# Kernel optimization log

Hardware: AMD Instinct MI355X
Metric: run time of the kernel (lower is better)

The kernel has to match this reference:

```python
import jax, jax.numpy as jnp
import numpy as np

HIDDEN = 512


def setup_inputs() -> dict:
    key = jax.random.key(0)
    k1, k2, k3, k4, k5 = jax.random.split(key, 5)
    scale = 1.0 / np.sqrt(HIDDEN)
    return {
        "decoder_hidden": jax.random.normal(k1, (64, HIDDEN), dtype=jnp.float32),
        "encoder_outputs": jax.random.normal(k2, (4096, 64, HIDDEN), dtype=jnp.float32),
        "W1": jax.random.uniform(k3, (HIDDEN, HIDDEN), jnp.float32, -scale, scale),
        "W2": jax.random.uniform(k4, (HIDDEN, HIDDEN), jnp.float32, -scale, scale),
        "v": jax.random.uniform(k5, (HIDDEN,), jnp.float32, -scale, scale),
    }


def reference(decoder_hidden, encoder_outputs, W1, W2, v):
    # decoder_hidden: (B, H); encoder_outputs: (S, B, H)
    enc = jnp.transpose(encoder_outputs, (1, 0, 2))          # (B, S, H)
    dec_proj = decoder_hidden @ W1.T                          # (B, H) — no need to repeat over S
    enc_proj = jnp.einsum('bsh,gh->bsg', enc, W2)             # (B, S, H)
    energy = jnp.tanh(dec_proj[:, None, :] + enc_proj) @ v    # (B, S)
    attn_weights = jax.nn.softmax(energy, axis=1)             # (B, S)
    context = jnp.einsum('bs,bsh->bh', attn_weights, enc)     # (B, H)
    return (context, attn_weights)
```

## Files before the change

kernel.cpp:

```cpp
#include <hip/hip_runtime.h>
#include <math.h>


#define BATCH 64
#define SEQ   4096
#define HID   512

typedef __attribute__((ext_vector_type(8))) short bf16x8;
typedef __attribute__((ext_vector_type(4))) float f32x4;

__device__ __forceinline__ float fast_tanh(float x) {
    return 1.0f - 2.0f / (__expf(2.0f * x) + 1.0f);
}

__device__ __forceinline__ unsigned cvt2(float lo, float hi) {
    unsigned r;
    asm("v_cvt_pk_bf16_f32 %0, %1, %2" : "=v"(r) : "v"(lo), "v"(hi));
    return r;
}

__device__ __forceinline__ void lds_barrier() {
    asm volatile("s_waitcnt lgkmcnt(0)" ::: "memory");
    __builtin_amdgcn_s_barrier();
}

__global__ void k_cvtW2(const float* __restrict__ W2, ushort* __restrict__ W2t)
{
    const int n  = blockIdx.x * 256 + threadIdx.x;
    const int g  = n >> 6, kc = n & 63;
    const int kb = kc >> 2, rgl = kc & 3;
    const int gh = g >> 8, wv = (g >> 6) & 3, fn = (g >> 4) & 3, gl = g & 15;

    const float* src = W2 + (size_t)g * HID + kc * 8;
    const float4 x = *reinterpret_cast<const float4*>(src);
    const float4 y = *reinterpret_cast<const float4*>(src + 4);
    uint4 u;
    u.x = cvt2(x.x, x.y);  u.y = cvt2(x.z, x.w);
    u.z = cvt2(y.x, y.y);  u.w = cvt2(y.z, y.w);

    const size_t dst = (size_t)gh * 131072 + kb * 8192 + wv * 2048 + fn * 512
                     + (rgl * 16 + gl) * 8;
    *reinterpret_cast<uint4*>(W2t + dst) = u;
}

__global__ void k_decproj(const float* __restrict__ dh,
                          const float* __restrict__ W1,
                          float* __restrict__ dp)
{
    __shared__ float wrow[HID];
    const int g = blockIdx.x;
    const int t = threadIdx.x;
    for (int i = t; i < HID; i += 256) wrow[i] = W1[g * HID + i];
    __syncthreads();

    const int b = t >> 2, q = t & 3;
    const float* dhb = dh + b * HID + q * 128;
    const float* wr  = wrow + q * 128;
    float acc = 0.f;
    #pragma unroll 8
    for (int i = 0; i < 128; i += 4) {
        const float4 d4 = *reinterpret_cast<const float4*>(dhb + i);
        acc = fmaf(d4.x, wr[i + 0], acc);
        acc = fmaf(d4.y, wr[i + 1], acc);
        acc = fmaf(d4.z, wr[i + 2], acc);
        acc = fmaf(d4.w, wr[i + 3], acc);
    }
    acc += __shfl_xor(acc, 1);
    acc += __shfl_xor(acc, 2);
    if (q == 0) dp[b * HID + g] = acc;
}

#define LDA 40

__global__ __launch_bounds__(256, 4)
void k_energy(const float* __restrict__ enc, const ushort* __restrict__ W2t,
              const float* __restrict__ dp,  const float* __restrict__ v,
              float* __restrict__ eparts)
{
    __shared__ __align__(16) ushort As[2][64 * LDA];
    __shared__ float part[4][64];

    const int idx  = blockIdx.x;
    const int g16  = idx >> 4, rr = idx & 15;
    const int gh   = rr >> 3;
    const int pair = (g16 << 3) | (rr & 7);
    const int schunk = pair & 63;
    const int b      = pair >> 6;
    const int s0     = schunk * 64;

    const int t    = threadIdx.x;
    const int lane = t & 63;
    const int wv   = t >> 6;
    const int gl   = lane & 15, rg = lane >> 4;

    f32x4 acc[4][4];
    const f32x4 z = {0.f, 0.f, 0.f, 0.f};
    #pragma unroll
    for (int m = 0; m < 4; ++m)
        #pragma unroll
        for (int n = 0; n < 4; ++n) acc[m][n] = z;

    const int arow = t >> 2, akq = t & 3;
    const float* aptr = enc + ((size_t)(s0 + arow) * BATCH + b) * HID + akq * 8;
    ushort* Aw0 = &As[0][arow * LDA + akq * 8];
    ushort* Aw1 = &As[1][arow * LDA + akq * 8];

    const ushort* Ap0 = &As[0][gl * LDA + rg * 8];
    const ushort* Ap1 = &As[1][gl * LDA + rg * 8];

    const ushort* bptr = W2t + (size_t)gh * 131072 + wv * 2048 + lane * 8;

    float4 a0 = *reinterpret_cast<const float4*>(aptr);
    float4 a1 = *reinterpret_cast<const float4*>(aptr + 4);
    {
        uint4 aw;
        aw.x = cvt2(a0.x, a0.y);  aw.y = cvt2(a0.z, a0.w);
        aw.z = cvt2(a1.x, a1.y);  aw.w = cvt2(a1.z, a1.w);
        *reinterpret_cast<uint4*>(Aw0) = aw;
    }
    a0 = *reinterpret_cast<const float4*>(aptr + 32);
    a1 = *reinterpret_cast<const float4*>(aptr + 36);
    lds_barrier();

    #pragma unroll
    for (int kb = 0; kb < 16; ++kb) {
        bf16x8 bfr[4];
        #pragma unroll
        for (int n = 0; n < 4; ++n)
            bfr[n] = *reinterpret_cast<const bf16x8*>(bptr + kb * 8192 + n * 512);

        const ushort* Ap = (kb & 1) ? Ap1 : Ap0;
        bf16x8 af[4];
        #pragma unroll
        for (int m = 0; m < 4; ++m)
            af[m] = *reinterpret_cast<const bf16x8*>(Ap + m * 16 * LDA);

        if (kb < 15) {
            uint4 aw;
            aw.x = cvt2(a0.x, a0.y);  aw.y = cvt2(a0.z, a0.w);
            aw.z = cvt2(a1.x, a1.y);  aw.w = cvt2(a1.z, a1.w);
            *reinterpret_cast<uint4*>((kb & 1) ? Aw0 : Aw1) = aw;
        }
        if (kb < 14) {
            a0 = *reinterpret_cast<const float4*>(aptr + (kb + 2) * 32);
            a1 = *reinterpret_cast<const float4*>(aptr + (kb + 2) * 32 + 4);
        }

        #pragma unroll
        for (int m = 0; m < 4; ++m)
            #pragma unroll
            for (int n = 0; n < 4; ++n)
                acc[m][n] = __builtin_amdgcn_mfma_f32_16x16x32_bf16(
                    af[m], bfr[n], acc[m][n], 0, 0, 0);

        lds_barrier();
    }

    float dpv[4], vv[4];
    #pragma unroll
    for (int n = 0; n < 4; ++n) {
        const int g = gh * 256 + wv * 64 + n * 16 + gl;
        dpv[n] = dp[b * HID + g];
        vv[n]  = v[g];
    }
    float p[4][4];
    #pragma unroll
    for (int m = 0; m < 4; ++m)
        #pragma unroll
        for (int r = 0; r < 4; ++r) p[m][r] = 0.f;
    #pragma unroll
    for (int n = 0; n < 4; ++n)
        #pragma unroll
        for (int m = 0; m < 4; ++m)
            #pragma unroll
            for (int r = 0; r < 4; ++r)
                p[m][r] += fast_tanh(dpv[n] + acc[m][n][r]) * vv[n];

    #pragma unroll
    for (int m = 0; m < 4; ++m)
        #pragma unroll
        for (int r = 0; r < 4; ++r) {
            float x = p[m][r];
            x += __shfl_xor(x, 1);
            x += __shfl_xor(x, 2);
            x += __shfl_xor(x, 4);
            x += __shfl_xor(x, 8);
            p[m][r] = x;
        }
    if (gl == 0) {
        #pragma unroll
        for (int m = 0; m < 4; ++m)
            #pragma unroll
            for (int r = 0; r < 4; ++r)
                part[wv][m * 16 + rg * 4 + r] = p[m][r];
    }
    __syncthreads();

    if (t < 64) {
        const float e = part[0][t] + part[1][t] + part[2][t] + part[3][t];
        eparts[(size_t)gh * BATCH * SEQ + (size_t)b * SEQ + s0 + t] = e;
    }
}

__global__ void k_softmax(const float* __restrict__ eparts,
                          float* __restrict__ attn)
{
    __shared__ float redm[4], reds[4];
    const int b = blockIdx.x, t = threadIdx.x;
    const float* e0 = eparts + (size_t)b * SEQ;
    const float* e1 = eparts + (size_t)BATCH * SEQ + (size_t)b * SEQ;

    float4 ev[4];
    float m = -3.4e38f;
    #pragma unroll
    for (int i = 0; i < 4; ++i) {
        const float4 x = *reinterpret_cast<const float4*>(e0 + i * 1024 + t * 4);
        const float4 y = *reinterpret_cast<const float4*>(e1 + i * 1024 + t * 4);
        ev[i] = make_float4(x.x + y.x, x.y + y.y, x.z + y.z, x.w + y.w);
        m = fmaxf(m, fmaxf(fmaxf(ev[i].x, ev[i].y), fmaxf(ev[i].z, ev[i].w)));
    }
    #pragma unroll
    for (int off = 1; off < 64; off <<= 1) m = fmaxf(m, __shfl_xor(m, off));
    if ((t & 63) == 0) redm[t >> 6] = m;
    __syncthreads();
    m = fmaxf(fmaxf(redm[0], redm[1]), fmaxf(redm[2], redm[3]));

    float s = 0.f;
    #pragma unroll
    for (int i = 0; i < 4; ++i) {
        ev[i].x = __expf(ev[i].x - m);  ev[i].y = __expf(ev[i].y - m);
        ev[i].z = __expf(ev[i].z - m);  ev[i].w = __expf(ev[i].w - m);
        s += (ev[i].x + ev[i].y) + (ev[i].z + ev[i].w);
    }
    #pragma unroll
    for (int off = 1; off < 64; off <<= 1) s += __shfl_xor(s, off);
    if ((t & 63) == 0) reds[t >> 6] = s;
    __syncthreads();
    s = (reds[0] + reds[1]) + (reds[2] + reds[3]);
    const float inv = 1.0f / s;

    float* o = attn + (size_t)b * SEQ;
    #pragma unroll
    for (int i = 0; i < 4; ++i) {
        const float4 w4 = make_float4(ev[i].x * inv, ev[i].y * inv,
                                      ev[i].z * inv, ev[i].w * inv);
        *reinterpret_cast<float4*>(o + i * 1024 + t * 4) = w4;
    }
}

__global__ void k_ctxpart(const float* __restrict__ enc,
                          const float* __restrict__ attn,
                          float* __restrict__ pctx)
{
    __shared__ float w[256];
    const int b  = blockIdx.x;
    const int sp = blockIdx.y;
    const int t  = threadIdx.x;

    w[t] = attn[(size_t)b * SEQ + sp * 256 + t];
    __syncthreads();

    const float2* e2 = reinterpret_cast<const float2*>(enc);
    size_t idx = ((size_t)sp * 256 * BATCH + b) * (HID / 2) + t;
    const size_t stride = (size_t)BATCH * (HID / 2);

    float ax = 0.f, ay = 0.f;
    #pragma unroll 4
    for (int s = 0; s < 256; ++s) {
        const float2 ev = e2[idx];
        const float ws = w[s];
        ax = fmaf(ws, ev.x, ax);
        ay = fmaf(ws, ev.y, ay);
        idx += stride;
    }
    float2* p2 = reinterpret_cast<float2*>(pctx);
    p2[((size_t)sp * BATCH + b) * (HID / 2) + t] = make_float2(ax, ay);
}

__global__ void k_ctxsum(const float* __restrict__ pctx,
                         float* __restrict__ ctx)
{
    const int i = blockIdx.x * 256 + threadIdx.x;
    float s = 0.f;
    #pragma unroll
    for (int sp = 0; sp < 16; ++sp) s += pctx[(size_t)sp * BATCH * HID + i];
    ctx[i] = s;
}

extern "C" void kernel_launch(void* const* d_in, const int* in_sizes, int n_in,
                              void* d_out, int out_size, void* d_ws, size_t ws_size,
                              hipStream_t stream)
{
    const float* dh  = (const float*)d_in[0];
    const float* enc = (const float*)d_in[1];
    const float* W1  = (const float*)d_in[2];
    const float* W2  = (const float*)d_in[3];
    const float* v   = (const float*)d_in[4];

    float* out  = (float*)d_out;
    float* ctx  = out;
    float* attn = out + BATCH * HID;

    float*  dp      = (float*)d_ws;
    ushort* W2t     = (ushort*)(dp + BATCH * HID);
    float*  shared2 = (float*)(W2t + HID * HID);
    float*  eparts  = shared2;
    float*  pctx    = shared2;

    k_cvtW2  <<<128, 256, 0, stream>>>(W2, W2t);
    k_decproj<<<HID, 256, 0, stream>>>(dh, W1, dp);
    k_energy <<<8192, 256, 0, stream>>>(enc, W2t, dp, v, eparts);
    k_softmax<<<BATCH, 256, 0, stream>>>(eparts, attn);
    k_ctxpart<<<dim3(BATCH, 16), 256, 0, stream>>>(enc, attn, pctx);
    k_ctxsum <<<BATCH * HID / 256, 256, 0, stream>>>(pctx, ctx);
}
```

Measured before the change: 328.8 us.

## Software-pipeline energy GEMM with register double-buffered fragments and deeper prefetch

Restructures the k_energy main loop so the W2 fragments and LDS A fragments for the next k-block are loaded into double-buffered registers before the MFMAs of the current block run. Global prefetch of encoder rows moves one step further ahead, and the barrier now sits before the next-fragment LDS read instead of after the MFMAs. The goal is to hide global and LDS load latency behind MFMA work. The extra register buffers raise register pressure, so launch bounds drop from 4 to 3 blocks per SM, which lowers occupancy.

Measured after the change: 347.4 us. 1.06x slower.

```diff
diff --git a/kernel.cpp b/kernel.cpp
--- a/kernel.cpp
+++ b/kernel.cpp
@@ -72,7 +72,7 @@
 
 #define LDA 40
 
-__global__ __launch_bounds__(256, 4)
+__global__ __launch_bounds__(256, 3)
 void k_energy(const float* __restrict__ enc, const ushort* __restrict__ W2t,
               const float* __restrict__ dp,  const float* __restrict__ v,
               float* __restrict__ eparts)
@@ -110,40 +110,56 @@
 
     const ushort* bptr = W2t + (size_t)gh * 131072 + wv * 2048 + lane * 8;
 
-    float4 a0 = *reinterpret_cast<const float4*>(aptr);
-    float4 a1 = *reinterpret_cast<const float4*>(aptr + 4);
+    bf16x8 af[2][4], bfr[2][4];
+    float4 ar[2][2];
+
     {
+        const float4 p0 = *reinterpret_cast<const float4*>(aptr);
+        const float4 p1 = *reinterpret_cast<const float4*>(aptr + 4);
         uint4 aw;
-        aw.x = cvt2(a0.x, a0.y);  aw.y = cvt2(a0.z, a0.w);
-        aw.z = cvt2(a1.x, a1.y);  aw.w = cvt2(a1.z, a1.w);
+        aw.x = cvt2(p0.x, p0.y);  aw.y = cvt2(p0.z, p0.w);
+        aw.z = cvt2(p1.x, p1.y);  aw.w = cvt2(p1.z, p1.w);
         *reinterpret_cast<uint4*>(Aw0) = aw;
     }
-    a0 = *reinterpret_cast<const float4*>(aptr + 32);
-    a1 = *reinterpret_cast<const float4*>(aptr + 36);
+    #pragma unroll
+    for (int n = 0; n < 4; ++n)
+        bfr[0][n] = *reinterpret_cast<const bf16x8*>(bptr + n * 512);
+    ar[0][0] = *reinterpret_cast<const float4*>(aptr + 32);
+    ar[0][1] = *reinterpret_cast<const float4*>(aptr + 36);
+    ar[1][0] = *reinterpret_cast<const float4*>(aptr + 64);
+    ar[1][1] = *reinterpret_cast<const float4*>(aptr + 68);
     lds_barrier();
+    #pragma unroll
+    for (int m = 0; m < 4; ++m)
+        af[0][m] = *reinterpret_cast<const bf16x8*>(Ap0 + m * 16 * LDA);
 
     #pragma unroll
     for (int kb = 0; kb < 16; ++kb) {
-        bf16x8 bfr[4];
-        #pragma unroll
-        for (int n = 0; n < 4; ++n)
-            bfr[n] = *reinterpret_cast<const bf16x8*>(bptr + kb * 8192 + n * 512);
-
-        const ushort* Ap = (kb & 1) ? Ap1 : Ap0;
-        bf16x8 af[4];
-        #pragma unroll
-        for (int m = 0; m < 4; ++m)
-            af[m] = *reinterpret_cast<const bf16x8*>(Ap + m * 16 * LDA);
+        const int cur = kb & 1, nxt = cur ^ 1;
 
         if (kb < 15) {
+            const float4 p0 = ar[cur][0], p1 = ar[cur][1];
             uint4 aw;
-            aw.x = cvt2(a0.x, a0.y);  aw.y = cvt2(a0.z, a0.w);
-            aw.z = cvt2(a1.x, a1.y);  aw.w = cvt2(a1.z, a1.w);
-            *reinterpret_cast<uint4*>((kb & 1) ? Aw0 : Aw1) = aw;
+            aw.x = cvt2(p0.x, p0.y);  aw.y = cvt2(p0.z, p0.w);
+            aw.z = cvt2(p1.x, p1.y);  aw.w = cvt2(p1.z, p1.w);
+            *reinterpret_cast<uint4*>(nxt ? Aw1 : Aw0) = aw;
+            #pragma unroll
+            for (int n = 0; n < 4; ++n)
+                bfr[nxt][n] = *reinterpret_cast<const bf16x8*>(
+                    bptr + (kb + 1) * 8192 + n * 512);
         }
         if (kb < 14) {
-            a0 = *reinterpret_cast<const float4*>(aptr + (kb + 2) * 32);
-            a1 = *reinterpret_cast<const float4*>(aptr + (kb + 2) * 32 + 4);
+            ar[cur][0] = *reinterpret_cast<const float4*>(aptr + (kb + 3) * 32);
+            ar[cur][1] = *reinterpret_cast<const float4*>(aptr + (kb + 3) * 32 + 4);
+        }
+
+        lds_barrier();
+
+        if (kb < 15) {
+            const ushort* Apn = nxt ? Ap1 : Ap0;
+            #pragma unroll
+            for (int m = 0; m < 4; ++m)
+                af[nxt][m] = *reinterpret_cast<const bf16x8*>(Apn + m * 16 * LDA);
         }
 
         #pragma unroll
@@ -151,9 +167,7 @@
             #pragma unroll
             for (int n = 0; n < 4; ++n)
                 acc[m][n] = __builtin_amdgcn_mfma_f32_16x16x32_bf16(
-                    af[m], bfr[n], acc[m][n], 0, 0, 0);
-
-        lds_barrier();
+                    af[cur][m], bfr[cur][n], acc[m][n], 0, 0, 0);
     }
 
     float dpv[4], vv[4];
```
